# Kernel optimization log

Measured on AMD Instinct MI355X. Metric: run time of the kernel, lower is better.

Reference implementation:

```python
import jax, jax.numpy as jnp
import numpy as np

D = 1024
H = 16
DK = D // H

def setup_inputs() -> dict:
    key = jax.random.key(0)
    k1, k2, k3 = jax.random.split(key, 3)
    x = jax.random.normal(k1, (2, 2048, D), dtype=jnp.float32)
    # torch nn.Linear weight shapes: qkv [3D, D], o [D, D]; y = x @ W.T
    scale = 1.0 / np.sqrt(D)
    W_qkv = jax.random.normal(k2, (3 * D, D), dtype=jnp.float32) * scale
    W_o = jax.random.normal(k3, (D, D), dtype=jnp.float32) * scale
    return {"x": x, "W_qkv": W_qkv, "W_o": W_o}

def reference(x, W_qkv, W_o):
    B, T, _ = x.shape
    qkv = x @ W_qkv.T                                    # [B, T, 3D]
    qkv = qkv.reshape(B, T, 3, H, DK)
    qkv = jnp.transpose(qkv, (0, 3, 2, 1, 4))            # [B, H, 3, T, DK]
    q, k, v = qkv[:, :, 0], qkv[:, :, 1], qkv[:, :, 2]   # each [B, H, T, DK]
    scores = jnp.einsum("bhqd,bhkd->bhqk", q, k) / np.sqrt(DK)
    causal = jnp.tril(jnp.ones((T, T), dtype=bool))       # keep lower triangle
    scores = jnp.where(causal, scores, -jnp.inf)
    attn = jax.nn.softmax(scores, axis=-1)
    out = jnp.einsum("bhqk,bhkd->bhqd", attn, v)          # [B, H, T, DK]
    out = jnp.transpose(out, (0, 2, 1, 3)).reshape(B, T, H * DK)
    return out @ W_o.T
```

## Files before the change

### kernel.cpp

```cpp
#include <hip/hip_runtime.h>
#include <hip/hip_bf16.h>

typedef __bf16 bf16x8 __attribute__((ext_vector_type(8)));
typedef float f32x4 __attribute__((ext_vector_type(4)));
typedef unsigned int u32;
typedef u32 u32x4 __attribute__((ext_vector_type(4)));

#define MFMA(a, b, c) __builtin_amdgcn_mfma_f32_16x16x32_bf16((a), (b), (c), 0, 0, 0)

static __device__ __forceinline__ bf16x8 ld8(const __bf16* p) {
  return *reinterpret_cast<const bf16x8*>(p);
}

static __device__ __forceinline__ u32 pkbf(float a, float b) {
  union { __bf16 h; unsigned short s; } x, y;
  x.h = (__bf16)a; y.h = (__bf16)b;
  return (u32)x.s | ((u32)y.s << 16);
}

typedef unsigned int __attribute__((address_space(1))) gu32_t;
typedef unsigned int __attribute__((address_space(3))) lu32_t;
static __device__ __forceinline__ void gld16(const __bf16* g, __bf16* l) {
  __builtin_amdgcn_global_load_lds((const gu32_t*)(const void*)g,
                                   (lu32_t*)(void*)l, 16, 0, 0);
}

__global__ __launch_bounds__(256)
void cvt_f32_bf16(const float* __restrict__ a, __bf16* __restrict__ oa, int na,
                  const float* __restrict__ b, __bf16* __restrict__ ob) {
  const int i = blockIdx.x * 256 + threadIdx.x;
  const float* src; __bf16* dst; int e;
  if (i < (na >> 3)) { src = a; dst = oa; e = i << 3; }
  else { src = b; dst = ob; e = (i << 3) - na; }
  f32x4 v0 = *reinterpret_cast<const f32x4*>(src + e);
  f32x4 v1 = *reinterpret_cast<const f32x4*>(src + e + 4);
  bf16x8 o;
#pragma unroll
  for (int j = 0; j < 4; ++j) { o[j] = (__bf16)v0[j]; o[j + 4] = (__bf16)v1[j]; }
  *reinterpret_cast<bf16x8*>(dst + e) = o;
}

static __device__ __forceinline__ void stage16f(__bf16* __restrict__ dst,
                                                const float* __restrict__ src) {
#pragma unroll
  for (int j = 0; j < 2; ++j) {
    f32x4 a = *reinterpret_cast<const f32x4*>(src + j * 8);
    f32x4 b = *reinterpret_cast<const f32x4*>(src + j * 8 + 4);
    bf16x8 o;
#pragma unroll
    for (int i = 0; i < 4; ++i) { o[i] = (__bf16)a[i]; o[i + 4] = (__bf16)b[i]; }
    *reinterpret_cast<bf16x8*>(dst + j * 8) = o;
  }
}

template<bool SPLIT, bool OUT_BF16, bool B_F32>
__global__ __launch_bounds__(256, 2)
void gemm_bt2(const __bf16* __restrict__ A, const void* __restrict__ Wv,
              void* __restrict__ Cv, __bf16* __restrict__ VT,
              int M, int N, int K) {
  __shared__ __bf16 lA[128 * 32];
  __shared__ __bf16 lB[128 * 32];

  const int tid = threadIdx.x;
  const int ntiles = N >> 7;
  const int mt = blockIdx.x / ntiles;
  const int nt = blockIdx.x % ntiles;
  const int m0 = mt << 7, n0 = nt << 7;
  const int lane = tid & 63, w = tid >> 6;
  const int wm = (w >> 1) << 6;
  const int wn = (w & 1) << 6;
  const int fr = lane & 15, fg = lane >> 4;

  f32x4 acc[4][4] = {};

  for (int k0 = 0; k0 < K; k0 += 32) {
    __syncthreads();
#pragma unroll
    for (int j = 0; j < 2; ++j) {
      const int c = (w << 1) | j;
      const int u = (c << 6) | lane;
      const int row = u >> 2, col = (u & 3) << 3;
      gld16(A + (size_t)(m0 + row) * K + k0 + col, lA + (c << 9));
    }
    if constexpr (B_F32) {
      const int srow = tid >> 1, scol = (tid & 1) << 4;
      stage16f(lB + srow * 32 + scol,
               (const float*)Wv + (size_t)(n0 + srow) * K + k0 + scol);
    } else {
#pragma unroll
      for (int j = 0; j < 2; ++j) {
        const int c = (w << 1) | j;
        const int u = (c << 6) | lane;
        const int row = u >> 2, col = (u & 3) << 3;
        gld16((const __bf16*)Wv + (size_t)(n0 + row) * K + k0 + col, lB + (c << 9));
      }
    }
    __syncthreads();

    bf16x8 af[4], bfr[4];
#pragma unroll
    for (int m = 0; m < 4; ++m)
      af[m] = ld8(lA + (wm + m * 16 + fr) * 32 + fg * 8);
#pragma unroll
    for (int n = 0; n < 4; ++n)
      bfr[n] = ld8(lB + (wn + n * 16 + fr) * 32 + fg * 8);
#pragma unroll
    for (int m = 0; m < 4; ++m)
#pragma unroll
      for (int n = 0; n < 4; ++n)
        acc[m][n] = MFMA(af[m], bfr[n], acc[m][n]);
  }

#pragma unroll
  for (int m = 0; m < 4; ++m) {
#pragma unroll
    for (int n = 0; n < 4; ++n) {
#pragma unroll
      for (int r = 0; r < 4; ++r) {
        int row = m0 + wm + m * 16 + fg * 4 + r;
        int col = n0 + wn + n * 16 + fr;
        if constexpr (SPLIT) {
          int b = row >> 11, t = row & 2047;
          if (col >= 2048) {
            VT[((size_t)(b << 10) + (col - 2048)) * 2048 + t] = (__bf16)acc[m][n][r];
          } else {
            ((__bf16*)Cv)[(size_t)row * 2048 + col] = (__bf16)acc[m][n][r];
          }
        } else if constexpr (OUT_BF16) {
          ((__bf16*)Cv)[(size_t)row * N + col] = (__bf16)acc[m][n][r];
        } else {
          ((float*)Cv)[(size_t)row * N + col] = acc[m][n][r];
        }
      }
    }
  }
}

__global__ __launch_bounds__(256, 4)
void attn_causal6(const __bf16* __restrict__ qk, const __bf16* __restrict__ vt,
                  __bf16* __restrict__ out) {
  constexpr float SC2 = 0.125f * 1.4426950408889634f;
  constexpr float NEG = -1e30f;

  __shared__ __bf16 lK[2][4096];
  __shared__ __bf16 lV[2][4096];

  const int tid = threadIdx.x;
  const int lane = tid & 63, w = tid >> 6;
  const int fr = lane & 15, fg = lane >> 4;
  const int blk = blockIdx.x;
  const int j = blk >> 3;
  const int bh = ((blk & 7) << 2) | (j & 3);
  const int qb = 31 - (j >> 2);
  const int b = bh >> 4, h = bh & 15;
  const int q0w = (qb << 6) + (w << 4);
  const int hoff = h * 64;
  const size_t qkbase = (size_t)b * (2048 * 2048);
  const __bf16* kb = qk + qkbase + 1024 + hoff;
  const __bf16* vtb = vt + (size_t)((b << 10) | hoff) * 2048;

  bf16x8 qf[2];
#pragma unroll
  for (int c = 0; c < 2; ++c)
    qf[c] = ld8(qk + qkbase + (size_t)(q0w + fr) * 2048 + hoff + c * 32 + fg * 8);

  f32x4 o[4] = {};
  float m = NEG;
  float l = 0.f;

#define STAGE(bf, k0s)                                                        \
  do {                                                                        \
    _Pragma("unroll")                                                         \
    for (int jj = 0; jj < 2; ++jj) {                                          \
      const int q = (w << 1) | jj;                                            \
      const int v = (q << 6) | lane;                                          \
      const int row = v >> 3;                                                 \
      const int cc = (v & 7) ^ (row & 7);                                     \
      gld16(kb + (size_t)((k0s) + row) * 2048 + (cc << 3), &lK[bf][q << 9]);  \
      gld16(vtb + (size_t)row * 2048 + (k0s) + (cc << 3), &lV[bf][q << 9]);   \
    }                                                                         \
  } while (0)

  int buf = 0;
  STAGE(0, 0);
  __syncthreads();

  for (int kt = 0; kt <= qb; ++kt) {
    const int k0 = kt << 6;
    if (kt < qb) STAGE(buf ^ 1, k0 + 64);

    f32x4 s[4] = {};
#pragma unroll
    for (int c = 0; c < 2; ++c) {
      bf16x8 kfc[4];
#pragma unroll
      for (int n = 0; n < 4; ++n) {
        const int row = n * 16 + fr;
        const int sc = ((c << 2) | fg) ^ (row & 7);
        kfc[n] = ld8(&lK[buf][(row << 6) + (sc << 3)]);
      }
#pragma unroll
      for (int n = 0; n < 4; ++n)
        s[n] = MFMA(kfc[n], qf[c], s[n]);
    }

    const bool diag = (kt == qb);
    float sv[4][4];
#pragma unroll
    for (int n = 0; n < 4; ++n)
#pragma unroll
      for (int r = 0; r < 4; ++r) {
        float x = s[n][r] * SC2;
        if (diag && (k0 + n * 16 + fg * 4 + r > q0w + fr)) x = NEG;
        sv[n][r] = x;
      }

    float t0 = fmaxf(fmaxf(sv[0][0], sv[0][1]), fmaxf(sv[0][2], sv[0][3]));
    float t1 = fmaxf(fmaxf(sv[1][0], sv[1][1]), fmaxf(sv[1][2], sv[1][3]));
    float t2 = fmaxf(fmaxf(sv[2][0], sv[2][1]), fmaxf(sv[2][2], sv[2][3]));
    float t3 = fmaxf(fmaxf(sv[3][0], sv[3][1]), fmaxf(sv[3][2], sv[3][3]));
    float rm = fmaxf(fmaxf(t0, t1), fmaxf(t2, t3));
    rm = fmaxf(rm, __shfl_xor(rm, 16));
    rm = fmaxf(rm, __shfl_xor(rm, 32));

    if (!__all(rm <= m + 16.f)) {
      float mnew = fmaxf(m, rm);
      float alpha = __builtin_exp2f(m - mnew);
      m = mnew;
      l *= alpha;
      float ao[4];
#pragma unroll
      for (int r = 0; r < 4; ++r)
        ao[r] = __shfl(alpha, fg * 4 + r);
#pragma unroll
      for (int n = 0; n < 4; ++n)
#pragma unroll
        for (int r = 0; r < 4; ++r)
          o[n][r] *= ao[r];
    }

    float p[4][4];
#pragma unroll
    for (int n = 0; n < 4; ++n)
#pragma unroll
      for (int r = 0; r < 4; ++r)
        p[n][r] = __builtin_exp2f(sv[n][r] - m);

    float u0 = (p[0][0] + p[0][1]) + (p[0][2] + p[0][3]);
    float u1 = (p[1][0] + p[1][1]) + (p[1][2] + p[1][3]);
    float u2 = (p[2][0] + p[2][1]) + (p[2][2] + p[2][3]);
    float u3 = (p[3][0] + p[3][1]) + (p[3][2] + p[3][3]);
    float rs = (u0 + u1) + (u2 + u3);
    rs += __shfl_xor(rs, 16);
    rs += __shfl_xor(rs, 32);
    l += rs;

    u32 wpk[4][2];
#pragma unroll
    for (int n = 0; n < 4; ++n) {
      wpk[n][0] = pkbf(p[n][0], p[n][1]);
      wpk[n][1] = pkbf(p[n][2], p[n][3]);
    }

    u32 rcv[2][2][2];
#pragma unroll
    for (int e = 0; e < 2; ++e) {
      const int src = fr + ((((fg & 1) << 1) | ((fg >> 1) ^ e)) << 4);
      const bool tsel = ((fg & 1) ^ e) != 0;
#pragma unroll
      for (int c = 0; c < 2; ++c)
#pragma unroll
        for (int hh = 0; hh < 2; ++hh) {
          u32 v = tsel ? wpk[(c << 1) | 1][hh] : wpk[(c << 1) | 0][hh];
          rcv[e][c][hh] = (u32)__shfl((int)v, src);
        }
    }
    const bool hi = (fg >> 1) != 0;
    u32x4 w0, w1;
#pragma unroll
    for (int a = 0; a < 2; ++a)
#pragma unroll
      for (int hh = 0; hh < 2; ++hh) {
        w0[2 * a + hh] = hi ? rcv[a ^ 1][0][hh] : rcv[a][0][hh];
        w1[2 * a + hh] = hi ? rcv[a ^ 1][1][hh] : rcv[a][1][hh];
      }
    bf16x8 pa[2];
    pa[0] = __builtin_bit_cast(bf16x8, w0);
    pa[1] = __builtin_bit_cast(bf16x8, w1);

#pragma unroll
    for (int c = 0; c < 2; ++c) {
      bf16x8 vfc[4];
#pragma unroll
      for (int n = 0; n < 4; ++n) {
        const int row = n * 16 + fr;
        const int sc = ((c << 2) | fg) ^ (row & 7);
        vfc[n] = ld8(&lV[buf][(row << 6) + (sc << 3)]);
      }
#pragma unroll
      for (int n = 0; n < 4; ++n)
        o[n] = MFMA(pa[c], vfc[n], o[n]);
    }

    __syncthreads();
    buf ^= 1;
  }
#undef STAGE

  float linv = 1.f / l;
  float lo[4];
#pragma unroll
  for (int r = 0; r < 4; ++r)
    lo[r] = __shfl(linv, fg * 4 + r);
#pragma unroll
  for (int n = 0; n < 4; ++n)
#pragma unroll
    for (int r = 0; r < 4; ++r) {
      int t = q0w + fg * 4 + r;
      out[((size_t)(b * 2048 + t)) * 1024 + hoff + n * 16 + fr] = (__bf16)(o[n][r] * lo[r]);
    }
}

extern "C" void kernel_launch(void* const* d_in, const int* in_sizes, int n_in,
                              void* d_out, int out_size, void* d_ws, size_t ws_size,
                              hipStream_t stream) {
  const float* x = (const float*)d_in[0];
  const float* w_qkv = (const float*)d_in[1];
  const float* w_o = (const float*)d_in[2];
  float* out = (float*)d_out;

  const int M = 4096;
  __bf16* qk = (__bf16*)d_ws;
  __bf16* vt = (__bf16*)((char*)d_ws + (size_t)M * 2048 * 2);
  __bf16* attn = (__bf16*)((char*)d_ws + (size_t)M * 3072 * 2);

  __bf16* xb = (__bf16*)d_out;
  __bf16* wqb = xb + 4194304;
  const int NX = 4194304;

  cvt_f32_bf16<<<3584, 256, 0, stream>>>(x, xb, NX, w_qkv, wqb);

  gemm_bt2<true, true, false><<<(M / 128) * (3072 / 128), 256, 0, stream>>>(
      xb, (const void*)wqb, (void*)qk, vt, M, 3072, 1024);

  attn_causal6<<<1024, 256, 0, stream>>>(qk, vt, attn);

  gemm_bt2<false, false, true><<<(M / 128) * (1024 / 128), 256, 0, stream>>>(
      attn, (const void*)w_o, (void*)out, nullptr, M, 1024, 1024);
}
```

Before: 137.0 us.

## Pair causal query blocks per workgroup, widen GEMM K-tile with swizzled LDS

Each attention workgroup now handles two query blocks, a long one and its mirrored short one, so both share the staged K/V tiles and the causal load is balanced. The grid halves to 512 blocks, with occupancy lowered to 2 to fit the extra registers. The GEMMs now stage 64-wide K tiles into an XOR-swizzled LDS layout to cut barrier count and bank conflicts. The output projection uses 64-wide N tiles for more blocks. The softmax scale is folded into Q in the QKV GEMM epilogue, which trades extra register pressure for less per-step attention arithmetic.

```diff
diff --git a/kernel.cpp b/kernel.cpp
--- a/kernel.cpp
+++ b/kernel.cpp
@@ -40,106 +40,227 @@
   *reinterpret_cast<bf16x8*>(dst + e) = o;
 }
 
-static __device__ __forceinline__ void stage16f(__bf16* __restrict__ dst,
-                                                const float* __restrict__ src) {
-#pragma unroll
-  for (int j = 0; j < 2; ++j) {
-    f32x4 a = *reinterpret_cast<const f32x4*>(src + j * 8);
-    f32x4 b = *reinterpret_cast<const f32x4*>(src + j * 8 + 4);
-    bf16x8 o;
-#pragma unroll
-    for (int i = 0; i < 4; ++i) { o[i] = (__bf16)a[i]; o[i + 4] = (__bf16)b[i]; }
-    *reinterpret_cast<bf16x8*>(dst + j * 8) = o;
-  }
-}
-
-template<bool SPLIT, bool OUT_BF16, bool B_F32>
+static __device__ __forceinline__ void stage8f(__bf16* __restrict__ dst,
+                                               const float* __restrict__ src) {
+  f32x4 a = *reinterpret_cast<const f32x4*>(src);
+  f32x4 b = *reinterpret_cast<const f32x4*>(src + 4);
+  bf16x8 o;
+#pragma unroll
+  for (int i = 0; i < 4; ++i) { o[i] = (__bf16)a[i]; o[i + 4] = (__bf16)b[i]; }
+  *reinterpret_cast<bf16x8*>(dst) = o;
+}
+
+template<int BN, bool SPLIT, bool OUT_BF16, bool B_F32>
 __global__ __launch_bounds__(256, 2)
-void gemm_bt2(const __bf16* __restrict__ A, const void* __restrict__ Wv,
-              void* __restrict__ Cv, __bf16* __restrict__ VT,
-              int M, int N, int K) {
-  __shared__ __bf16 lA[128 * 32];
-  __shared__ __bf16 lB[128 * 32];
+void gemm3(const __bf16* __restrict__ A, const void* __restrict__ Wv,
+           void* __restrict__ Cv, __bf16* __restrict__ VT,
+           int M, int N, int K) {
+  constexpr int NF = BN / 32;
+  constexpr float SC2Q = 0.125f * 1.4426950408889634f;
+  __shared__ __bf16 lA[128 * 64];
+  __shared__ __bf16 lB[BN * 64];
 
   const int tid = threadIdx.x;
-  const int ntiles = N >> 7;
+  const int ntiles = N / BN;
   const int mt = blockIdx.x / ntiles;
   const int nt = blockIdx.x % ntiles;
-  const int m0 = mt << 7, n0 = nt << 7;
+  const int m0 = mt << 7, n0 = nt * BN;
   const int lane = tid & 63, w = tid >> 6;
   const int wm = (w >> 1) << 6;
-  const int wn = (w & 1) << 6;
+  const int wn = (w & 1) * (BN / 2);
   const int fr = lane & 15, fg = lane >> 4;
 
-  f32x4 acc[4][4] = {};
-
-  for (int k0 = 0; k0 < K; k0 += 32) {
+  f32x4 acc[4][NF] = {};
+
+  for (int k0 = 0; k0 < K; k0 += 64) {
     __syncthreads();
 #pragma unroll
-    for (int j = 0; j < 2; ++j) {
-      const int c = (w << 1) | j;
-      const int u = (c << 6) | lane;
-      const int row = u >> 2, col = (u & 3) << 3;
-      gld16(A + (size_t)(m0 + row) * K + k0 + col, lA + (c << 9));
+    for (int jj = 0; jj < 4; ++jj) {
+      const int q = (w << 2) | jj;
+      const int v = (q << 6) | lane;
+      const int row = v >> 3;
+      const int cc = (v & 7) ^ (row & 7);
+      gld16(A + (size_t)(m0 + row) * K + k0 + (cc << 3), lA + (q << 9));
     }
     if constexpr (B_F32) {
-      const int srow = tid >> 1, scol = (tid & 1) << 4;
-      stage16f(lB + srow * 32 + scol,
-               (const float*)Wv + (size_t)(n0 + srow) * K + k0 + scol);
+#pragma unroll
+      for (int hh = 0; hh < BN / 64; ++hh) {
+        const int row = (tid >> 2) + (hh << 6);
+        const int c0 = (tid & 3) << 1;
+        const float* src = (const float*)Wv + (size_t)(n0 + row) * K + k0 + (c0 << 3);
+#pragma unroll
+        for (int cg = 0; cg < 2; ++cg)
+          stage8f(lB + (row << 6) + (((c0 + cg) ^ (row & 7)) << 3), src + (cg << 3));
+      }
     } else {
 #pragma unroll
-      for (int j = 0; j < 2; ++j) {
-        const int c = (w << 1) | j;
-        const int u = (c << 6) | lane;
-        const int row = u >> 2, col = (u & 3) << 3;
-        gld16((const __bf16*)Wv + (size_t)(n0 + row) * K + k0 + col, lB + (c << 9));
+      for (int jj = 0; jj < NF; ++jj) {
+        const int q = w * NF + jj;
+        const int v = (q << 6) | lane;
+        const int row = v >> 3;
+        const int cc = (v & 7) ^ (row & 7);
+        gld16((const __bf16*)Wv + (size_t)(n0 + row) * K + k0 + (cc << 3), lB + (q << 9));
       }
     }
     __syncthreads();
 
-    bf16x8 af[4], bfr[4];
-#pragma unroll
-    for (int m = 0; m < 4; ++m)
-      af[m] = ld8(lA + (wm + m * 16 + fr) * 32 + fg * 8);
-#pragma unroll
-    for (int n = 0; n < 4; ++n)
-      bfr[n] = ld8(lB + (wn + n * 16 + fr) * 32 + fg * 8);
-#pragma unroll
-    for (int m = 0; m < 4; ++m)
-#pragma unroll
-      for (int n = 0; n < 4; ++n)
-        acc[m][n] = MFMA(af[m], bfr[n], acc[m][n]);
+    bf16x8 af[2][4], bfr[2][NF];
+#pragma unroll
+    for (int kc = 0; kc < 2; ++kc) {
+#pragma unroll
+      for (int m = 0; m < 4; ++m) {
+        const int row = wm + m * 16 + fr;
+        af[kc][m] = ld8(lA + (row << 6) + ((((kc << 2) | fg) ^ (row & 7)) << 3));
+      }
+#pragma unroll
+      for (int n = 0; n < NF; ++n) {
+        const int row = wn + n * 16 + fr;
+        bfr[kc][n] = ld8(lB + (row << 6) + ((((kc << 2) | fg) ^ (row & 7)) << 3));
+      }
+    }
+#pragma unroll
+    for (int kc = 0; kc < 2; ++kc)
+#pragma unroll
+      for (int m = 0; m < 4; ++m)
+#pragma unroll
+        for (int n = 0; n < NF; ++n)
+          acc[m][n] = MFMA(af[kc][m], bfr[kc][n], acc[m][n]);
   }
 
 #pragma unroll
   for (int m = 0; m < 4; ++m) {
 #pragma unroll
-    for (int n = 0; n < 4; ++n) {
+    for (int n = 0; n < NF; ++n) {
 #pragma unroll
       for (int r = 0; r < 4; ++r) {
         int row = m0 + wm + m * 16 + fg * 4 + r;
         int col = n0 + wn + n * 16 + fr;
+        float v = acc[m][n][r];
         if constexpr (SPLIT) {
           int b = row >> 11, t = row & 2047;
           if (col >= 2048) {
-            VT[((size_t)(b << 10) + (col - 2048)) * 2048 + t] = (__bf16)acc[m][n][r];
+            VT[((size_t)(b << 10) + (col - 2048)) * 2048 + t] = (__bf16)v;
           } else {
-            ((__bf16*)Cv)[(size_t)row * 2048 + col] = (__bf16)acc[m][n][r];
+            if (col < 1024) v *= SC2Q;
+            ((__bf16*)Cv)[(size_t)row * 2048 + col] = (__bf16)v;
           }
         } else if constexpr (OUT_BF16) {
-          ((__bf16*)Cv)[(size_t)row * N + col] = (__bf16)acc[m][n][r];
+          ((__bf16*)Cv)[(size_t)row * N + col] = (__bf16)v;
         } else {
-          ((float*)Cv)[(size_t)row * N + col] = acc[m][n][r];
+          ((float*)Cv)[(size_t)row * N + col] = v;
         }
       }
     }
   }
 }
 
-__global__ __launch_bounds__(256, 4)
-void attn_causal6(const __bf16* __restrict__ qk, const __bf16* __restrict__ vt,
+static __device__ __forceinline__ void softmax_step(
+    f32x4 (&s)[4], f32x4 (&o)[4], float& m, float& l, bf16x8 (&pa)[2],
+    bool diag, int q0wt, int k0, int fg, int fr) {
+  constexpr float NEG = -1e30f;
+  float sv[4][4];
+#pragma unroll
+  for (int n = 0; n < 4; ++n)
+#pragma unroll
+    for (int r = 0; r < 4; ++r) {
+      float x = s[n][r];
+      if (diag && (k0 + n * 16 + fg * 4 + r > q0wt + fr)) x = NEG;
+      sv[n][r] = x;
+    }
+
+  float t0 = fmaxf(fmaxf(sv[0][0], sv[0][1]), fmaxf(sv[0][2], sv[0][3]));
+  float t1 = fmaxf(fmaxf(sv[1][0], sv[1][1]), fmaxf(sv[1][2], sv[1][3]));
+  float t2 = fmaxf(fmaxf(sv[2][0], sv[2][1]), fmaxf(sv[2][2], sv[2][3]));
+  float t3 = fmaxf(fmaxf(sv[3][0], sv[3][1]), fmaxf(sv[3][2], sv[3][3]));
+  float rm = fmaxf(fmaxf(t0, t1), fmaxf(t2, t3));
+  rm = fmaxf(rm, __shfl_xor(rm, 16));
+  rm = fmaxf(rm, __shfl_xor(rm, 32));
+
+  if (!__all(rm <= m + 16.f)) {
+    float mnew = fmaxf(m, rm);
+    float alpha = __builtin_exp2f(m - mnew);
+    m = mnew;
+    l *= alpha;
+    float ao[4];
+#pragma unroll
+    for (int r = 0; r < 4; ++r)
+      ao[r] = __shfl(alpha, fg * 4 + r);
+#pragma unroll
+    for (int n = 0; n < 4; ++n)
+#pragma unroll
+      for (int r = 0; r < 4; ++r)
+        o[n][r] *= ao[r];
+  }
+
+  float p[4][4];
+#pragma unroll
+  for (int n = 0; n < 4; ++n)
+#pragma unroll
+    for (int r = 0; r < 4; ++r)
+      p[n][r] = __builtin_exp2f(sv[n][r] - m);
+
+  float u0 = (p[0][0] + p[0][1]) + (p[0][2] + p[0][3]);
+  float u1 = (p[1][0] + p[1][1]) + (p[1][2] + p[1][3]);
+  float u2 = (p[2][0] + p[2][1]) + (p[2][2] + p[2][3]);
+  float u3 = (p[3][0] + p[3][1]) + (p[3][2] + p[3][3]);
+  float rs = (u0 + u1) + (u2 + u3);
+  rs += __shfl_xor(rs, 16);
+  rs += __shfl_xor(rs, 32);
+  l += rs;
+
+  u32 wpk[4][2];
+#pragma unroll
+  for (int n = 0; n < 4; ++n) {
+    wpk[n][0] = pkbf(p[n][0], p[n][1]);
+    wpk[n][1] = pkbf(p[n][2], p[n][3]);
+  }
+
+  u32 rcv[2][2][2];
+#pragma unroll
+  for (int e = 0; e < 2; ++e) {
+    const int src = fr + ((((fg & 1) << 1) | ((fg >> 1) ^ e)) << 4);
+    const bool tsel = ((fg & 1) ^ e) != 0;
+#pragma unroll
+    for (int c = 0; c < 2; ++c)
+#pragma unroll
+      for (int hh = 0; hh < 2; ++hh) {
+        u32 v = tsel ? wpk[(c << 1) | 1][hh] : wpk[(c << 1) | 0][hh];
+        rcv[e][c][hh] = (u32)__shfl((int)v, src);
+      }
+  }
+  const bool hi = (fg >> 1) != 0;
+  u32x4 w0, w1;
+#pragma unroll
+  for (int a = 0; a < 2; ++a)
+#pragma unroll
+    for (int hh = 0; hh < 2; ++hh) {
+      w0[2 * a + hh] = hi ? rcv[a ^ 1][0][hh] : rcv[a][0][hh];
+      w1[2 * a + hh] = hi ? rcv[a ^ 1][1][hh] : rcv[a][1][hh];
+    }
+  pa[0] = __builtin_bit_cast(bf16x8, w0);
+  pa[1] = __builtin_bit_cast(bf16x8, w1);
+}
+
+static __device__ __forceinline__ void write_out(
+    __bf16* __restrict__ out, f32x4 (&o)[4], float l,
+    int b, int hoff, int q0wt, int fg, int fr) {
+  float linv = 1.f / l;
+  float lo[4];
+#pragma unroll
+  for (int r = 0; r < 4; ++r)
+    lo[r] = __shfl(linv, fg * 4 + r);
+#pragma unroll
+  for (int n = 0; n < 4; ++n)
+#pragma unroll
+    for (int r = 0; r < 4; ++r) {
+      int t = q0wt + fg * 4 + r;
+      out[((size_t)(b * 2048 + t)) * 1024 + hoff + n * 16 + fr] = (__bf16)(o[n][r] * lo[r]);
+    }
+}
+
+__global__ __launch_bounds__(256, 2)
+void attn_causal7(const __bf16* __restrict__ qk, const __bf16* __restrict__ vt,
                   __bf16* __restrict__ out) {
-  constexpr float SC2 = 0.125f * 1.4426950408889634f;
   constexpr float NEG = -1e30f;
 
   __shared__ __bf16 lK[2][4096];
@@ -149,24 +270,27 @@
   const int lane = tid & 63, w = tid >> 6;
   const int fr = lane & 15, fg = lane >> 4;
   const int blk = blockIdx.x;
-  const int j = blk >> 3;
-  const int bh = ((blk & 7) << 2) | (j & 3);
-  const int qb = 31 - (j >> 2);
+  const int rest = blk >> 3;
+  const int bh = ((blk & 7) << 2) | (rest & 3);
+  const int i = rest >> 2;
+  const int qb0 = 31 - i, qb1 = i;
   const int b = bh >> 4, h = bh & 15;
-  const int q0w = (qb << 6) + (w << 4);
+  const int q0w0 = (qb0 << 6) + (w << 4);
+  const int q0w1 = (qb1 << 6) + (w << 4);
   const int hoff = h * 64;
   const size_t qkbase = (size_t)b * (2048 * 2048);
   const __bf16* kb = qk + qkbase + 1024 + hoff;
   const __bf16* vtb = vt + (size_t)((b << 10) | hoff) * 2048;
 
-  bf16x8 qf[2];
-#pragma unroll
-  for (int c = 0; c < 2; ++c)
-    qf[c] = ld8(qk + qkbase + (size_t)(q0w + fr) * 2048 + hoff + c * 32 + fg * 8);
-
-  f32x4 o[4] = {};
-  float m = NEG;
-  float l = 0.f;
+  bf16x8 qf0[2], qf1[2];
+#pragma unroll
+  for (int c = 0; c < 2; ++c) {
+    qf0[c] = ld8(qk + qkbase + (size_t)(q0w0 + fr) * 2048 + hoff + c * 32 + fg * 8);
+    qf1[c] = ld8(qk + qkbase + (size_t)(q0w1 + fr) * 2048 + hoff + c * 32 + fg * 8);
+  }
+
+  f32x4 o0[4] = {}, o1[4] = {};
+  float m_0 = NEG, l_0 = 0.f, m_1 = NEG, l_1 = 0.f;
 
 #define STAGE(bf, k0s)                                                        \
   do {                                                                        \
@@ -185,11 +309,12 @@
   STAGE(0, 0);
   __syncthreads();
 
-  for (int kt = 0; kt <= qb; ++kt) {
+  for (int kt = 0; kt <= qb0; ++kt) {
     const int k0 = kt << 6;
-    if (kt < qb) STAGE(buf ^ 1, k0 + 64);
-
-    f32x4 s[4] = {};
+    if (kt < qb0) STAGE(buf ^ 1, k0 + 64);
+    const bool act1 = (kt <= qb1);
+
+    f32x4 s0[4] = {}, s1[4] = {};
 #pragma unroll
     for (int c = 0; c < 2; ++c) {
       bf16x8 kfc[4];
@@ -201,92 +326,18 @@
       }
 #pragma unroll
       for (int n = 0; n < 4; ++n)
-        s[n] = MFMA(kfc[n], qf[c], s[n]);
-    }
-
-    const bool diag = (kt == qb);
-    float sv[4][4];
-#pragma unroll
-    for (int n = 0; n < 4; ++n)
-#pragma unroll
-      for (int r = 0; r < 4; ++r) {
-        float x = s[n][r] * SC2;
-        if (diag && (k0 + n * 16 + fg * 4 + r > q0w + fr)) x = NEG;
-        sv[n][r] = x;
-      }
-
-    float t0 = fmaxf(fmaxf(sv[0][0], sv[0][1]), fmaxf(sv[0][2], sv[0][3]));
-    float t1 = fmaxf(fmaxf(sv[1][0], sv[1][1]), fmaxf(sv[1][2], sv[1][3]));
-    float t2 = fmaxf(fmaxf(sv[2][0], sv[2][1]), fmaxf(sv[2][2], sv[2][3]));
-    float t3 = fmaxf(fmaxf(sv[3][0], sv[3][1]), fmaxf(sv[3][2], sv[3][3]));
-    float rm = fmaxf(fmaxf(t0, t1), fmaxf(t2, t3));
-    rm = fmaxf(rm, __shfl_xor(rm, 16));
-    rm = fmaxf(rm, __shfl_xor(rm, 32));
-
-    if (!__all(rm <= m + 16.f)) {
-      float mnew = fmaxf(m, rm);
-      float alpha = __builtin_exp2f(m - mnew);
-      m = mnew;
-      l *= alpha;
-      float ao[4];
-#pragma unroll
-      for (int r = 0; r < 4; ++r)
-        ao[r] = __shfl(alpha, fg * 4 + r);
-#pragma unroll
-      for (int n = 0; n < 4; ++n)
-#pragma unroll
-        for (int r = 0; r < 4; ++r)
-          o[n][r] *= ao[r];
-    }
-
-    float p[4][4];
-#pragma unroll
-    for (int n = 0; n < 4; ++n)
-#pragma unroll
-      for (int r = 0; r < 4; ++r)
-        p[n][r] = __builtin_exp2f(sv[n][r] - m);
-
-    float u0 = (p[0][0] + p[0][1]) + (p[0][2] + p[0][3]);
-    float u1 = (p[1][0] + p[1][1]) + (p[1][2] + p[1][3]);
-    float u2 = (p[2][0] + p[2][1]) + (p[2][2] + p[2][3]);
-    float u3 = (p[3][0] + p[3][1]) + (p[3][2] + p[3][3]);
-    float rs = (u0 + u1) + (u2 + u3);
-    rs += __shfl_xor(rs, 16);
-    rs += __shfl_xor(rs, 32);
-    l += rs;
-
-    u32 wpk[4][2];
-#pragma unroll
-    for (int n = 0; n < 4; ++n) {
-      wpk[n][0] = pkbf(p[n][0], p[n][1]);
-      wpk[n][1] = pkbf(p[n][2], p[n][3]);
-    }
-
-    u32 rcv[2][2][2];
-#pragma unroll
-    for (int e = 0; e < 2; ++e) {
-      const int src = fr + ((((fg & 1) << 1) | ((fg >> 1) ^ e)) << 4);
-      const bool tsel = ((fg & 1) ^ e) != 0;
-#pragma unroll
-      for (int c = 0; c < 2; ++c)
-#pragma unroll
-        for (int hh = 0; hh < 2; ++hh) {
-          u32 v = tsel ? wpk[(c << 1) | 1][hh] : wpk[(c << 1) | 0][hh];
-          rcv[e][c][hh] = (u32)__shfl((int)v, src);
-        }
-    }
-    const bool hi = (fg >> 1) != 0;
-    u32x4 w0, w1;
-#pragma unroll
-    for (int a = 0; a < 2; ++a)
-#pragma unroll
-      for (int hh = 0; hh < 2; ++hh) {
-        w0[2 * a + hh] = hi ? rcv[a ^ 1][0][hh] : rcv[a][0][hh];
-        w1[2 * a + hh] = hi ? rcv[a ^ 1][1][hh] : rcv[a][1][hh];
-      }
-    bf16x8 pa[2];
-    pa[0] = __builtin_bit_cast(bf16x8, w0);
-    pa[1] = __builtin_bit_cast(bf16x8, w1);
+        s0[n] = MFMA(kfc[n], qf0[c], s0[n]);
+      if (act1) {
+#pragma unroll
+        for (int n = 0; n < 4; ++n)
+          s1[n] = MFMA(kfc[n], qf1[c], s1[n]);
+      }
+    }
+
+    bf16x8 pa0[2], pa1[2];
+    softmax_step(s0, o0, m_0, l_0, pa0, kt == qb0, q0w0, k0, fg, fr);
+    if (act1)
+      softmax_step(s1, o1, m_1, l_1, pa1, kt == qb1, q0w1, k0, fg, fr);
 
 #pragma unroll
     for (int c = 0; c < 2; ++c) {
@@ -299,7 +350,12 @@
       }
 #pragma unroll
       for (int n = 0; n < 4; ++n)
-        o[n] = MFMA(pa[c], vfc[n], o[n]);
+        o0[n] = MFMA(pa0[c], vfc[n], o0[n]);
+      if (act1) {
+#pragma unroll
+        for (int n = 0; n < 4; ++n)
+          o1[n] = MFMA(pa1[c], vfc[n], o1[n]);
+      }
     }
 
     __syncthreads();
@@ -307,18 +363,8 @@
   }
 #undef STAGE
 
-  float linv = 1.f / l;
-  float lo[4];
-#pragma unroll
-  for (int r = 0; r < 4; ++r)
-    lo[r] = __shfl(linv, fg * 4 + r);
-#pragma unroll
-  for (int n = 0; n < 4; ++n)
-#pragma unroll
-    for (int r = 0; r < 4; ++r) {
-      int t = q0w + fg * 4 + r;
-      out[((size_t)(b * 2048 + t)) * 1024 + hoff + n * 16 + fr] = (__bf16)(o[n][r] * lo[r]);
-    }
+  write_out(out, o0, l_0, b, hoff, q0w0, fg, fr);
+  write_out(out, o1, l_1, b, hoff, q0w1, fg, fr);
 }
 
 extern "C" void kernel_launch(void* const* d_in, const int* in_sizes, int n_in,
@@ -340,11 +386,11 @@
 
   cvt_f32_bf16<<<3584, 256, 0, stream>>>(x, xb, NX, w_qkv, wqb);
 
-  gemm_bt2<true, true, false><<<(M / 128) * (3072 / 128), 256, 0, stream>>>(
+  gemm3<128, true, true, false><<<(M / 128) * (3072 / 128), 256, 0, stream>>>(
       xb, (const void*)wqb, (void*)qk, vt, M, 3072, 1024);
 
-  attn_causal6<<<1024, 256, 0, stream>>>(qk, vt, attn);
-
-  gemm_bt2<false, false, true><<<(M / 128) * (1024 / 128), 256, 0, stream>>>(
+  attn_causal7<<<512, 256, 0, stream>>>(qk, vt, attn);
+
+  gemm3<64, false, false, true><<<(M / 128) * (1024 / 64), 256, 0, stream>>>(
       attn, (const void*)w_o, (void*)out, nullptr, M, 1024, 1024);
 }
```

After: 127.1 us. -7.2%, faster.
